# Kernel tuning notes

Measured on AMD Instinct MI355X. Metric: run time of the kernel, lower is better.

The kernel has to match this reference:

```python
import jax, jax.numpy as jnp
import numpy as np

N, E, F, H = 50000, 800000, 64, 4
NEG_SLOPE = 0.2
LN_EPS = 1e-5


def setup_inputs() -> dict:
    key = jax.random.key(0)
    ks = jax.random.split(key, 12)
    h = jax.random.normal(ks[0], (N, F), dtype=jnp.float32)
    src = jax.random.randint(ks[1], (E,), 0, N, dtype=jnp.int32)
    dst = jax.random.randint(ks[2], (E,), 0, N, dtype=jnp.int32)
    s = 1.0 / np.sqrt(F)
    fc_w = jax.random.uniform(ks[3], (F, H * F), jnp.float32, -s, s)
    attn_l = jax.random.normal(ks[4], (H, F), dtype=jnp.float32) * s
    attn_r = jax.random.normal(ks[5], (H, F), dtype=jnp.float32) * s
    gat_bias = jnp.zeros((H * F,), dtype=jnp.float32)
    so = 1.0 / np.sqrt(H * F)
    out_w = jax.random.uniform(ks[6], (H * F, F), jnp.float32, -so, so)
    out_b = jax.random.uniform(ks[7], (F,), jnp.float32, -so, so)
    ln_g = jnp.ones((F,), dtype=jnp.float32)
    ln_b = jnp.zeros((F,), dtype=jnp.float32)
    return {"h": h, "src": src, "dst": dst, "fc_w": fc_w, "attn_l": attn_l,
            "attn_r": attn_r, "gat_bias": gat_bias, "out_w": out_w,
            "out_b": out_b, "ln_g": ln_g, "ln_b": ln_b}


def reference(h, src, dst, fc_w, attn_l, attn_r, gat_bias, out_w, out_b, ln_g, ln_b):
    # --- GATConv (DGL semantics) ---
    feat = (h @ fc_w).reshape(N, H, F)                      # [N,H,F]
    el = jnp.einsum('nhf,hf->nh', feat, attn_l)             # [N,H]
    er = jnp.einsum('nhf,hf->nh', feat, attn_r)             # [N,H]
    e = jax.nn.leaky_relu(el[src] + er[dst], NEG_SLOPE)     # [E,H]
    # edge softmax over incoming edges of each dst node
    m = jax.ops.segment_max(e, dst, num_segments=N)         # [N,H]
    ex = jnp.exp(e - m[dst])                                # [E,H]
    z = jax.ops.segment_sum(ex, dst, num_segments=N)        # [N,H]
    alpha = ex / z[dst]                                     # [E,H]
    msg = feat[src] * alpha[:, :, None]                     # [E,H,F]
    rst = jax.ops.segment_sum(msg, dst, num_segments=N)     # [N,H,F]
    rst = rst + gat_bias.reshape(H, F)
    # --- out linear + layernorm ---
    x = rst.reshape(N, H * F) @ out_w + out_b               # [N,F]
    mu = jnp.mean(x, axis=-1, keepdims=True)
    var = jnp.var(x, axis=-1, keepdims=True)
    return (x - mu) * jax.lax.rsqrt(var + LN_EPS) * ln_g + ln_b
```

## Files before the change

### kernel.cpp

```cpp
#include <hip/hip_runtime.h>

#define NN 50000
#define EE 800000
#define FF 64
#define HH 4
#define HF 256
#define NEG_SLOPE 0.2f
#define LN_EPS 1e-5f
#define WPACK_N (4 * 8 * 64 * 8)
#define WPACKA_N (16 * 2 * 64 * 8)
#define NTILE (NN / 16)
#define TROW 264

typedef __attribute__((ext_vector_type(8))) short s8v;
typedef __attribute__((ext_vector_type(4))) float f4v;

__device__ __forceinline__ unsigned short f32_to_bf16_rne(float x) {
  unsigned int u = __float_as_uint(x);
  unsigned int r = u + 0x7FFFu + ((u >> 16) & 1u);
  return (unsigned short)(r >> 16);
}

__device__ __forceinline__ float readlane_f(float v, int l) {
  return __uint_as_float(
      (unsigned)__builtin_amdgcn_readlane((int)__float_as_uint(v), l));
}

__global__ __launch_bounds__(256) void k_prep(
    const float* __restrict__ fc_w, const float* __restrict__ out_w,
    unsigned short* __restrict__ wpackA, unsigned short* __restrict__ wpack,
    int* __restrict__ cnt) {
  const int idx = blockIdx.x * 256 + threadIdx.x;
  if (idx < WPACKA_N) {
    const int j = idx & 7;
    const int l = (idx >> 3) & 63;
    const int t = (idx >> 9) & 1;
    const int ct = idx >> 10;
    const int k = 32 * t + (l >> 4) * 8 + j;
    const int c = 16 * ct + (l & 15);
    wpackA[idx] = f32_to_bf16_rne(fc_w[k * HF + c]);
  } else if (idx < WPACKA_N + WPACK_N) {
    const int i2 = idx - WPACKA_N;
    const int j = i2 & 7;
    const int l = (i2 >> 3) & 63;
    const int t = (i2 >> 9) & 7;
    const int ct = i2 >> 12;
    const int k = 32 * t + (l >> 4) * 8 + j;
    const int c = 16 * ct + (l & 15);
    wpack[i2] = f32_to_bf16_rne(out_w[k * FF + c]);
  }
  if (idx < NN) cnt[idx] = 0;
}

__global__ __launch_bounds__(256) void k_feat(
    const float* __restrict__ h, const unsigned short* __restrict__ wpackA,
    const float* __restrict__ attn_l, const float* __restrict__ attn_r,
    unsigned short* __restrict__ featb, float* __restrict__ el,
    float* __restrict__ er) {
  __shared__ unsigned short wlds[WPACKA_N];
  {
    const uint4* s = (const uint4*)wpackA;
    uint4* d = (uint4*)wlds;
    for (int i = threadIdx.x; i < 2048; i += 256) d[i] = s[i];
  }
  __syncthreads();
  const int wave = threadIdx.x >> 6;
  const int lane = threadIdx.x & 63;
  const int tile = blockIdx.x * 4 + wave;
  if (tile >= NTILE) return;
  const int n0 = tile * 16;
  const int cl = lane & 15;
  const int quad = lane >> 4;

  float al[16], ar[16];
#pragma unroll
  for (int ct = 0; ct < 16; ++ct) {
    al[ct] = attn_l[16 * ct + cl];
    ar[ct] = attn_r[16 * ct + cl];
  }

  s8v a[2];
#pragma unroll
  for (int t = 0; t < 2; ++t) {
    const float* hp = h + (size_t)(n0 + cl) * FF + 32 * t + quad * 8;
    float hv[8];
    *(float4*)hv = *(const float4*)hp;
    *(float4*)(hv + 4) = *(const float4*)(hp + 4);
    s8v av;
#pragma unroll
    for (int i = 0; i < 8; ++i) av[i] = (short)f32_to_bf16_rne(hv[i]);
    a[t] = av;
  }

  f4v acc[16];
#pragma unroll
  for (int ct = 0; ct < 16; ++ct) {
    f4v z = {0.f, 0.f, 0.f, 0.f};
    acc[ct] = z;
#pragma unroll
    for (int t = 0; t < 2; ++t) {
      const s8v b = *(const s8v*)(wlds + ((ct * 2 + t) * 64 + lane) * 8);
      acc[ct] = __builtin_amdgcn_mfma_f32_16x16x32_bf16(a[t], b, acc[ct], 0, 0, 0);
    }
  }

#pragma unroll
  for (int r = 0; r < 4; ++r) {
    const int n = n0 + quad * 4 + r;
    float pl[4] = {0.f, 0.f, 0.f, 0.f};
    float pr[4] = {0.f, 0.f, 0.f, 0.f};
#pragma unroll
    for (int g = 0; g < 4; ++g) {
      const float x0 = acc[g][r];
      const float x1 = acc[g + 4][r];
      const float x2 = acc[g + 8][r];
      const float x3 = acc[g + 12][r];
      uint2 pk;
      pk.x = (unsigned)f32_to_bf16_rne(x0) | ((unsigned)f32_to_bf16_rne(x1) << 16);
      pk.y = (unsigned)f32_to_bf16_rne(x2) | ((unsigned)f32_to_bf16_rne(x3) << 16);
      *(uint2*)(featb + (size_t)n * HF + (16 * g + cl) * 4) = pk;
      pl[0] = fmaf(x0, al[g], pl[0]);      pr[0] = fmaf(x0, ar[g], pr[0]);
      pl[1] = fmaf(x1, al[g + 4], pl[1]);  pr[1] = fmaf(x1, ar[g + 4], pr[1]);
      pl[2] = fmaf(x2, al[g + 8], pl[2]);  pr[2] = fmaf(x2, ar[g + 8], pr[2]);
      pl[3] = fmaf(x3, al[g + 12], pl[3]); pr[3] = fmaf(x3, ar[g + 12], pr[3]);
    }
#pragma unroll
    for (int off = 1; off < 16; off <<= 1) {
#pragma unroll
      for (int hh = 0; hh < 4; ++hh) {
        pl[hh] += __shfl_xor(pl[hh], off, 64);
        pr[hh] += __shfl_xor(pr[hh], off, 64);
      }
    }
    if (cl == 0) {
      *(float4*)(el + (size_t)n * 4) = make_float4(pl[0], pl[1], pl[2], pl[3]);
      *(float4*)(er + (size_t)n * 4) = make_float4(pr[0], pr[1], pr[2], pr[3]);
    }
  }
}

__global__ void k_scatter(const int* __restrict__ src,
                          const int* __restrict__ dst,
                          int* __restrict__ cnt, int* __restrict__ colp) {
  int e = blockIdx.x * blockDim.x + threadIdx.x;
  if (e < EE) {
    const int d = dst[e];
    const int pos = atomicAdd(&cnt[d], 1);
    if (pos < 64) colp[(d << 6) | pos] = src[e];
  }
}

__global__ __launch_bounds__(256) void k_gather_out(
    const unsigned short* __restrict__ featb, const float* __restrict__ el,
    const float* __restrict__ er, const int* __restrict__ cnt,
    const int* __restrict__ colp, const float* __restrict__ gat_bias,
    const unsigned short* __restrict__ wpack, const float* __restrict__ out_b,
    const float* __restrict__ ln_g, const float* __restrict__ ln_b,
    float* __restrict__ out) {
  __shared__ unsigned short tile[16][TROW];
  const int wave = threadIdx.x >> 6;
  const int lane = threadIdx.x & 63;
  const int n0 = blockIdx.x * 16;
  const float gb0 = gat_bias[lane], gb1 = gat_bias[64 + lane];
  const float gb2 = gat_bias[128 + lane], gb3 = gat_bias[192 + lane];
  const unsigned short* fb = featb + lane * HH;

#pragma unroll
  for (int r = 0; r < 4; ++r) {
    const int row = wave * 4 + r;
    const int n = n0 + row;
    const int m = cnt[n];
    const float4 erv = *(const float4*)(er + (size_t)n * 4);
    float a0 = 0.f, a1 = 0.f, a2 = 0.f, a3 = 0.f;
    float z0 = 0.f, z1 = 0.f, z2 = 0.f, z3 = 0.f;
    float w0 = 0.f, w1 = 0.f, w2 = 0.f, w3 = 0.f;
    int s = 0;
    if (lane < m) {
      s = colp[(n << 6) | lane];
      const float4 elv = *(const float4*)(el + (size_t)s * 4);
      float e0 = elv.x + erv.x, e1 = elv.y + erv.y;
      float e2 = elv.z + erv.z, e3 = elv.w + erv.w;
      e0 = e0 > 0.f ? e0 : NEG_SLOPE * e0;
      e1 = e1 > 0.f ? e1 : NEG_SLOPE * e1;
      e2 = e2 > 0.f ? e2 : NEG_SLOPE * e2;
      e3 = e3 > 0.f ? e3 : NEG_SLOPE * e3;
      w0 = __expf(e0); w1 = __expf(e1);
      w2 = __expf(e2); w3 = __expf(e3);
    }
    for (int e = 0; e < m; e += 8) {
#pragma unroll
      for (int j = 0; j < 8; ++j) {
        const int le = e + j;
        const int se = __builtin_amdgcn_readlane(s, le);
        const float we0 = readlane_f(w0, le);
        const float we1 = readlane_f(w1, le);
        const float we2 = readlane_f(w2, le);
        const float we3 = readlane_f(w3, le);
        const uint2 d = *(const uint2*)(fb + (size_t)se * HF);
        z0 += we0; z1 += we1; z2 += we2; z3 += we3;
        a0 = fmaf(we0, __uint_as_float(d.x << 16), a0);
        a1 = fmaf(we1, __uint_as_float(d.x & 0xFFFF0000u), a1);
        a2 = fmaf(we2, __uint_as_float(d.y << 16), a2);
        a3 = fmaf(we3, __uint_as_float(d.y & 0xFFFF0000u), a3);
      }
    }
    tile[row][lane]       = f32_to_bf16_rne((z0 > 0.f ? a0 / z0 : 0.f) + gb0);
    tile[row][64 + lane]  = f32_to_bf16_rne((z1 > 0.f ? a1 / z1 : 0.f) + gb1);
    tile[row][128 + lane] = f32_to_bf16_rne((z2 > 0.f ? a2 / z2 : 0.f) + gb2);
    tile[row][192 + lane] = f32_to_bf16_rne((z3 > 0.f ? a3 / z3 : 0.f) + gb3);
  }
  __syncthreads();
  if (wave != 0) return;

  const int cl = lane & 15;
  const int quad = lane >> 4;
  s8v a[8];
#pragma unroll
  for (int t = 0; t < 8; ++t)
    a[t] = *(const s8v*)(&tile[cl][32 * t + quad * 8]);

  f4v acc[4];
#pragma unroll
  for (int ct = 0; ct < 4; ++ct) {
    f4v z = {0.f, 0.f, 0.f, 0.f};
    acc[ct] = z;
#pragma unroll
    for (int t = 0; t < 8; ++t) {
      const s8v b = *(const s8v*)(wpack + ((ct * 8 + t) * 64 + lane) * 8);
      acc[ct] = __builtin_amdgcn_mfma_f32_16x16x32_bf16(a[t], b, acc[ct], 0, 0, 0);
    }
  }

  float x[4][4];
  float s1[4], s2[4];
#pragma unroll
  for (int r = 0; r < 4; ++r) { s1[r] = 0.f; s2[r] = 0.f; }
#pragma unroll
  for (int ct = 0; ct < 4; ++ct) {
    const float ob = out_b[16 * ct + cl];
#pragma unroll
    for (int r = 0; r < 4; ++r) {
      const float v = acc[ct][r] + ob;
      x[ct][r] = v;
      s1[r] += v;
      s2[r] += v * v;
    }
  }
#pragma unroll
  for (int r = 0; r < 4; ++r) {
#pragma unroll
    for (int off = 1; off < 16; off <<= 1) {
      s1[r] += __shfl_xor(s1[r], off, 64);
      s2[r] += __shfl_xor(s2[r], off, 64);
    }
  }
#pragma unroll
  for (int r = 0; r < 4; ++r) {
    const float mu = s1[r] * (1.f / 64.f);
    const float var = s2[r] * (1.f / 64.f) - mu * mu;
    const float inv = rsqrtf(var + LN_EPS);
    const int row = n0 + quad * 4 + r;
#pragma unroll
    for (int ct = 0; ct < 4; ++ct) {
      const int c = 16 * ct + cl;
      out[(size_t)row * FF + c] = (x[ct][r] - mu) * inv * ln_g[c] + ln_b[c];
    }
  }
}

extern "C" void kernel_launch(void* const* d_in, const int* in_sizes, int n_in,
                              void* d_out, int out_size, void* d_ws,
                              size_t ws_size, hipStream_t stream) {
  const float* h_in   = (const float*)d_in[0];
  const int*   src    = (const int*)d_in[1];
  const int*   dst    = (const int*)d_in[2];
  const float* fc_w   = (const float*)d_in[3];
  const float* attn_l = (const float*)d_in[4];
  const float* attn_r = (const float*)d_in[5];
  const float* gbias  = (const float*)d_in[6];
  const float* out_w  = (const float*)d_in[7];
  const float* out_b  = (const float*)d_in[8];
  const float* ln_g   = (const float*)d_in[9];
  const float* ln_b   = (const float*)d_in[10];
  float* out = (float*)d_out;

  char* p = (char*)d_ws;
  auto alloc = [&](size_t bytes) {
    char* q = p;
    p += (bytes + 255) & ~(size_t)255;
    return q;
  };
  unsigned short* featb  = (unsigned short*)alloc((size_t)NN * HF * 2);
  unsigned short* wpack  = (unsigned short*)alloc((size_t)WPACK_N * 2);
  unsigned short* wpackA = (unsigned short*)alloc((size_t)WPACKA_N * 2);
  float* el      = (float*)alloc((size_t)NN * HH * 4);
  float* er      = (float*)alloc((size_t)NN * HH * 4);
  int*   cnt     = (int*)alloc((size_t)NN * 4);
  int*   colp    = (int*)alloc((size_t)NN * 64 * 4);

  k_prep<<<256, 256, 0, stream>>>(fc_w, out_w, wpackA, wpack, cnt);
  k_feat<<<(NTILE + 3) / 4, 256, 0, stream>>>(h_in, wpackA, attn_l, attn_r,
                                              featb, el, er);
  k_scatter<<<(EE + 255) / 256, 256, 0, stream>>>(src, dst, cnt, colp);
  k_gather_out<<<NTILE, 256, 0, stream>>>(featb, el, er, cnt, colp, gbias,
                                          wpack, out_b, ln_g, ln_b, out);
}
```

Before: 210.2 us.

## Fuse edge scatter into feature GEMM kernel and store neighbor lists as 16-bit

Merges the edge-bucketing scatter and the node feature projection into one launch, with block index ranges selecting the role, so the two independent phases overlap and a kernel boundary disappears. Neighbor index lists are stored as unsigned short, which halves their write and read traffic; this relies on node ids fitting in 16 bits. The projection weights are now read directly from global memory instead of being staged into LDS, which removes the LDS copy and barrier but relies on cache hits for repeated weight loads.

```diff
diff --git a/kernel.cpp b/kernel.cpp
--- a/kernel.cpp
+++ b/kernel.cpp
@@ -11,6 +11,8 @@
 #define WPACKA_N (16 * 2 * 64 * 8)
 #define NTILE (NN / 16)
 #define TROW 264
+#define SCAT_BLOCKS ((EE + 255) / 256)
+#define FEAT_BLOCKS ((NTILE + 3) / 4)
 
 typedef __attribute__((ext_vector_type(8))) short s8v;
 typedef __attribute__((ext_vector_type(4))) float f4v;
@@ -52,21 +54,25 @@
   if (idx < NN) cnt[idx] = 0;
 }
 
-__global__ __launch_bounds__(256) void k_feat(
+__global__ __launch_bounds__(256) void k_fs2(
+    const int* __restrict__ src, const int* __restrict__ dst,
+    int* __restrict__ cnt, unsigned short* __restrict__ colp,
     const float* __restrict__ h, const unsigned short* __restrict__ wpackA,
     const float* __restrict__ attn_l, const float* __restrict__ attn_r,
     unsigned short* __restrict__ featb, float* __restrict__ el,
     float* __restrict__ er) {
-  __shared__ unsigned short wlds[WPACKA_N];
-  {
-    const uint4* s = (const uint4*)wpackA;
-    uint4* d = (uint4*)wlds;
-    for (int i = threadIdx.x; i < 2048; i += 256) d[i] = s[i];
-  }
-  __syncthreads();
+  if (blockIdx.x < SCAT_BLOCKS) {
+    const int e = blockIdx.x * 256 + threadIdx.x;
+    if (e < EE) {
+      const int d = dst[e];
+      const int pos = atomicAdd(&cnt[d], 1);
+      if (pos < 64) colp[(d << 6) | pos] = (unsigned short)src[e];
+    }
+    return;
+  }
   const int wave = threadIdx.x >> 6;
   const int lane = threadIdx.x & 63;
-  const int tile = blockIdx.x * 4 + wave;
+  const int tile = (blockIdx.x - SCAT_BLOCKS) * 4 + wave;
   if (tile >= NTILE) return;
   const int n0 = tile * 16;
   const int cl = lane & 15;
@@ -99,7 +105,7 @@
     acc[ct] = z;
 #pragma unroll
     for (int t = 0; t < 2; ++t) {
-      const s8v b = *(const s8v*)(wlds + ((ct * 2 + t) * 64 + lane) * 8);
+      const s8v b = *(const s8v*)(wpackA + ((ct * 2 + t) * 64 + lane) * 8);
       acc[ct] = __builtin_amdgcn_mfma_f32_16x16x32_bf16(a[t], b, acc[ct], 0, 0, 0);
     }
   }
@@ -139,21 +145,11 @@
   }
 }
 
-__global__ void k_scatter(const int* __restrict__ src,
-                          const int* __restrict__ dst,
-                          int* __restrict__ cnt, int* __restrict__ colp) {
-  int e = blockIdx.x * blockDim.x + threadIdx.x;
-  if (e < EE) {
-    const int d = dst[e];
-    const int pos = atomicAdd(&cnt[d], 1);
-    if (pos < 64) colp[(d << 6) | pos] = src[e];
-  }
-}
-
 __global__ __launch_bounds__(256) void k_gather_out(
     const unsigned short* __restrict__ featb, const float* __restrict__ el,
     const float* __restrict__ er, const int* __restrict__ cnt,
-    const int* __restrict__ colp, const float* __restrict__ gat_bias,
+    const unsigned short* __restrict__ colp,
+    const float* __restrict__ gat_bias,
     const unsigned short* __restrict__ wpack, const float* __restrict__ out_b,
     const float* __restrict__ ln_g, const float* __restrict__ ln_b,
     float* __restrict__ out) {
@@ -176,7 +172,7 @@
     float w0 = 0.f, w1 = 0.f, w2 = 0.f, w3 = 0.f;
     int s = 0;
     if (lane < m) {
-      s = colp[(n << 6) | lane];
+      s = (int)colp[(n << 6) | lane];
       const float4 elv = *(const float4*)(el + (size_t)s * 4);
       float e0 = elv.x + erv.x, e1 = elv.y + erv.y;
       float e2 = elv.z + erv.z, e3 = elv.w + erv.w;
@@ -296,12 +292,11 @@
   float* el      = (float*)alloc((size_t)NN * HH * 4);
   float* er      = (float*)alloc((size_t)NN * HH * 4);
   int*   cnt     = (int*)alloc((size_t)NN * 4);
-  int*   colp    = (int*)alloc((size_t)NN * 64 * 4);
+  unsigned short* colp = (unsigned short*)alloc((size_t)NN * 64 * 2);
 
   k_prep<<<256, 256, 0, stream>>>(fc_w, out_w, wpackA, wpack, cnt);
-  k_feat<<<(NTILE + 3) / 4, 256, 0, stream>>>(h_in, wpackA, attn_l, attn_r,
-                                              featb, el, er);
-  k_scatter<<<(EE + 255) / 256, 256, 0, stream>>>(src, dst, cnt, colp);
+  k_fs2<<<SCAT_BLOCKS + FEAT_BLOCKS, 256, 0, stream>>>(
+      src, dst, cnt, colp, h_in, wpackA, attn_l, attn_r, featb, el, er);
   k_gather_out<<<NTILE, 256, 0, stream>>>(featb, el, er, cnt, colp, gbias,
                                           wpack, out_b, ln_g, ln_b, out);
 }
```

After: 223.1 us. 1.06x slower.
